# Performance work log

Hardware: AMD Instinct MI355X
Metric: run time of the kernel (lower is better)

The kernel has to match this reference:

```python
import jax, jax.numpy as jnp
import numpy as np


def setup_inputs() -> dict:
    key = jax.random.key(0)
    k1, k2 = jax.random.split(key)
    B, C, H, W = 32, 2, 512, 512
    inp = jax.random.normal(k1, (B, C, H, W), dtype=jnp.float32)
    tgt = jax.random.normal(k2, (B, C, H, W), dtype=jnp.float32)
    return {"input": inp, "target": tgt}


def reference(input, target):
    B, C, H, W = input.shape
    # normalized coordinate grids: (j+1)/W along x, (p+1)/H along y
    xg = jnp.arange(1, W + 1, dtype=input.dtype) / W  # (W,)
    yg = jnp.arange(1, H + 1, dtype=input.dtype) / H  # (H,)
    # softmax over flattened heatmap per (b, c)
    p = jax.nn.softmax(input.reshape(B, C, H * W), axis=-1).reshape(B, C, H, W)
    # soft-argmax coords in normalized units, then scaled to pixels (*W, *H)
    pred_x = jnp.einsum('bchw,w->bc', p, xg) * W
    pred_y = jnp.einsum('bchw,h->bc', p, yg) * H
    # ground truth: hard argmax of target heatmap -> pixel coords
    idx = jnp.argmax(target.reshape(B, C, H * W), axis=-1)
    true_x = (idx % W + 1).astype(input.dtype)   # ((idx%W+1)/W)*W
    true_y = (idx // W + 1).astype(input.dtype)  # ((idx//W+1)/H)*H
    ed = jnp.sqrt((true_x - pred_x) ** 2 + (true_y - pred_y) ** 2)  # (B, C)
    s_i = jnp.sum(ed[:, 0])   # channel 0 -> inferior
    s_s = jnp.sum(ed[:, 1:])  # remaining channels -> superior
    denom = jnp.asarray(B, input.dtype)
    return (s_i / denom, s_s / denom, (s_i + s_s) / denom)
```

## Files before the change

kernel.cpp:

```cpp
#include <hip/hip_runtime.h>
#include <math.h>

constexpr int Wd      = 512;
constexpr int Hd      = 512;
constexpr int HW      = Wd * Hd;
constexpr int NBC     = 64;
constexpr int SPLITS  = 32;
constexpr int CHUNK   = HW / SPLITS;
constexpr int NPART   = NBC * SPLITS;
constexpr int THREADS = 256;
constexpr int F4_PER_T = CHUNK / 4 / THREADS;


__global__ __launch_bounds__(THREADS) void dsnt_pass1(
    const float* __restrict__ inp, const float* __restrict__ tgt,
    float* __restrict__ ws) {
  const int bid   = blockIdx.x;
  const int role  = bid >> 11;
  const int sub   = bid & 2047;
  const int bc    = sub >> 5;
  const int split = sub & (SPLITS - 1);
  const int t     = threadIdx.x;
  const int rbase = split * CHUNK;

  __shared__ float sm0[4], sm1[4], sm2[4];
  __shared__ int   smi[4];
  const int wave = t >> 6;

  float* Pl = ws;
  float* Px = ws + NPART;
  float* Py = ws + 2 * NPART;
  float* Pv = ws + 3 * NPART;
  int*   Pi = (int*)(ws + 4 * NPART);

  if (role == 0) {
    const float4* ip4 = (const float4*)(inp + (size_t)bc * HW + (size_t)rbase);
    float4 a[F4_PER_T];
#pragma unroll
    for (int i = 0; i < F4_PER_T; ++i) a[i] = ip4[t + i * THREADS];

    float lA = 0.f, lB = 0.f, sxA = 0.f, sxB = 0.f, syA = 0.f, syB = 0.f;
#pragma unroll
    for (int i = 0; i < F4_PER_T; ++i) {
      const int r = rbase + (t + i * THREADS) * 4;
      const float yc = (float)((r >> 9) + 1);
      const float x0 = (float)((r & 511) + 1);
      const float e0 = __expf(a[i].x);
      const float e1 = __expf(a[i].y);
      const float e2 = __expf(a[i].z);
      const float e3 = __expf(a[i].w);
      lA += e0 + e2;
      lB += e1 + e3;
      sxA = fmaf(e0, x0,       sxA);  sxA = fmaf(e2, x0 + 2.f, sxA);
      sxB = fmaf(e1, x0 + 1.f, sxB);  sxB = fmaf(e3, x0 + 3.f, sxB);
      syA = fmaf(e0 + e2, yc, syA);
      syB = fmaf(e1 + e3, yc, syB);
    }
    float l = lA + lB, sx = sxA + sxB, sy = syA + syB;

#pragma unroll
    for (int off = 32; off; off >>= 1) {
      l  += __shfl_xor(l, off);
      sx += __shfl_xor(sx, off);
      sy += __shfl_xor(sy, off);
    }
    if ((t & 63) == 0) { sm0[wave] = l; sm1[wave] = sx; sm2[wave] = sy; }
    __syncthreads();
    if (t == 0) {
#pragma unroll
      for (int wv = 1; wv < 4; ++wv) { l += sm0[wv]; sx += sm1[wv]; sy += sm2[wv]; }
      Pl[sub] = l; Px[sub] = sx; Py[sub] = sy;
    }
  } else {
    const float4* tp4 = (const float4*)(tgt + (size_t)bc * HW + (size_t)rbase);
    float4 b[F4_PER_T];
#pragma unroll
    for (int i = 0; i < F4_PER_T; ++i) b[i] = tp4[t + i * THREADS];

    float tvA = -INFINITY, tvB = -INFINITY;
    int   tiA = 0, tiB = 0;
#pragma unroll
    for (int i = 0; i < F4_PER_T; ++i) {
      const int r = rbase + (t + i * THREADS) * 4;
      if (b[i].x > tvA) { tvA = b[i].x; tiA = r; }
      if (b[i].z > tvA) { tvA = b[i].z; tiA = r + 2; }
      if (b[i].y > tvB) { tvB = b[i].y; tiB = r + 1; }
      if (b[i].w > tvB) { tvB = b[i].w; tiB = r + 3; }
    }
    float tv = tvA; int ti = tiA;
    if (tvB > tv || (tvB == tv && tiB < ti)) { tv = tvB; ti = tiB; }

#pragma unroll
    for (int off = 32; off; off >>= 1) {
      const float tv2 = __shfl_xor(tv, off);
      const int   ti2 = __shfl_xor(ti, off);
      if (tv2 > tv || (tv2 == tv && ti2 < ti)) { tv = tv2; ti = ti2; }
    }
    if ((t & 63) == 0) { sm0[wave] = tv; smi[wave] = ti; }
    __syncthreads();
    if (t == 0) {
#pragma unroll
      for (int wv = 1; wv < 4; ++wv) {
        const float tv2 = sm0[wv];
        const int   ti2 = smi[wv];
        if (tv2 > tv || (tv2 == tv && ti2 < ti)) { tv = tv2; ti = ti2; }
      }
      Pv[sub] = tv; Pi[sub] = ti;
    }
  }
}

__global__ __launch_bounds__(256) void dsnt_pass2(const float* __restrict__ ws,
                                                  float* __restrict__ out) {
  const int t    = threadIdx.x;
  const int bc   = t >> 2;
  const int part = t & 3;
  const float* Pl = ws;
  const float* Px = ws + NPART;
  const float* Py = ws + 2 * NPART;
  const float* Pv = ws + 3 * NPART;
  const int*   Pi = (const int*)(ws + 4 * NPART);

  float l = 0.f, sx = 0.f, sy = 0.f;
  float tv = -INFINITY;
  int   ti = 0x7fffffff;
#pragma unroll
  for (int j = 0; j < 8; ++j) {
    const int p = bc * SPLITS + part * 8 + j;
    l  += Pl[p];
    sx += Px[p];
    sy += Py[p];
    const float v  = Pv[p];
    const int   ix = Pi[p];
    if (v > tv || (v == tv && ix < ti)) { tv = v; ti = ix; }
  }
#pragma unroll
  for (int off = 1; off <= 2; off <<= 1) {
    l  += __shfl_xor(l, off);
    sx += __shfl_xor(sx, off);
    sy += __shfl_xor(sy, off);
    const float tv2 = __shfl_xor(tv, off);
    const int   ti2 = __shfl_xor(ti, off);
    if (tv2 > tv || (tv2 == tv && ti2 < ti)) { tv = tv2; ti = ti2; }
  }

  __shared__ float edArr[NBC];
  if (part == 0) {
    const float predx = sx / l;
    const float predy = sy / l;
    const float truex = (float)((ti & 511) + 1);
    const float truey = (float)((ti >> 9) + 1);
    const float dx = truex - predx, dy = truey - predy;
    edArr[bc] = sqrtf(dx * dx + dy * dy);
  }
  __syncthreads();
  if (t < NBC) {
    const float ed = edArr[t];
    float ei = (t & 1) ? 0.f : ed;
    float es = (t & 1) ? ed : 0.f;
#pragma unroll
    for (int off = 32; off; off >>= 1) {
      ei += __shfl_xor(ei, off);
      es += __shfl_xor(es, off);
    }
    if (t == 0) {
      out[0] = ei * (1.f / 32.f);
      out[1] = es * (1.f / 32.f);
      out[2] = (ei + es) * (1.f / 32.f);
    }
  }
}

extern "C" void kernel_launch(void* const* d_in, const int* in_sizes, int n_in,
                              void* d_out, int out_size, void* d_ws, size_t ws_size,
                              hipStream_t stream) {
  const float* inp = (const float*)d_in[0];
  const float* tgt = (const float*)d_in[1];
  float* out = (float*)d_out;
  float* ws  = (float*)d_ws;

  dsnt_pass1<<<2 * NPART, THREADS, 0, stream>>>(inp, tgt, ws);
  dsnt_pass2<<<1, 256, 0, stream>>>(ws, out);
}
```

Baseline: 148.0 us.

## Stream pass1 through LDS with double-buffered direct global-to-LDS loads per wave

Each wave now owns an 8192-element segment and streams it through a per-wave double buffer in LDS using global_load_lds, with manual waitcnt to overlap the next chunk's load with compute on the current one. Each wave writes its own partial result, so the block-level shared reduction and barrier go away, and the grid shrinks to 1024 blocks. The aim is more bytes in flight per wave and fewer, larger work items, at the cost of hand-coded waitcnt encodings that depend on correct ordering.

```diff
diff --git a/kernel.cpp b/kernel.cpp
--- a/kernel.cpp
+++ b/kernel.cpp
@@ -5,27 +5,47 @@
 constexpr int Hd      = 512;
 constexpr int HW      = Wd * Hd;
 constexpr int NBC     = 64;
-constexpr int SPLITS  = 32;
-constexpr int CHUNK   = HW / SPLITS;
+constexpr int SEG     = 8192;
+constexpr int SPLITS  = HW / SEG;
 constexpr int NPART   = NBC * SPLITS;
 constexpr int THREADS = 256;
-constexpr int F4_PER_T = CHUNK / 4 / THREADS;
+constexpr int CHUNKF  = 1024;
+constexpr int NCHUNK  = SEG / CHUNKF;
 
+
+typedef __attribute__((address_space(1))) const void gvoid_t;
+typedef __attribute__((address_space(3))) void lvoid_t;
+
+#define WAIT_VM4()   __builtin_amdgcn_s_waitcnt(0x0F74)
+#define WAIT_VM0()   __builtin_amdgcn_s_waitcnt(0x0F70)
+#define WAIT_LGKM0() __builtin_amdgcn_s_waitcnt(0xC07F)
+
+__device__ __forceinline__ void stage_chunk(const float* __restrict__ g,
+                                            float* l, int lane) {
+#pragma unroll
+  for (int j = 0; j < 4; ++j) {
+    __builtin_amdgcn_global_load_lds((gvoid_t*)(g + j * 256 + lane * 4),
+                                     (lvoid_t*)(l + j * 256), 16, 0, 0);
+  }
+}
 
 __global__ __launch_bounds__(THREADS) void dsnt_pass1(
     const float* __restrict__ inp, const float* __restrict__ tgt,
     float* __restrict__ ws) {
-  const int bid   = blockIdx.x;
-  const int role  = bid >> 11;
-  const int sub   = bid & 2047;
-  const int bc    = sub >> 5;
-  const int split = sub & (SPLITS - 1);
-  const int t     = threadIdx.x;
-  const int rbase = split * CHUNK;
+  __shared__ __align__(16) float lds[2][4][CHUNKF];
+  const int t    = threadIdx.x;
+  const int lane = t & 63;
+  const int wv   = t >> 6;
+  const int bid  = blockIdx.x;
+  const int role = bid >> 9;
+  const int wid  = ((bid & 511) << 2) | wv;
+  const int bc    = wid >> 5;
+  const int split = wid & (SPLITS - 1);
+  const int hbase = split * SEG;
 
-  __shared__ float sm0[4], sm1[4], sm2[4];
-  __shared__ int   smi[4];
-  const int wave = t >> 6;
+  const float* src = (role == 0 ? inp : tgt) + (size_t)bc * HW + hbase;
+  float* lbuf0 = &lds[0][wv][0];
+  float* lbuf1 = &lds[1][wv][0];
 
   float* Pl = ws;
   float* Px = ws + NPART;
@@ -33,80 +53,75 @@
   float* Pv = ws + 3 * NPART;
   int*   Pi = (int*)(ws + 4 * NPART);
 
+  stage_chunk(src, lbuf0, lane);
+  stage_chunk(src + CHUNKF, lbuf1, lane);
+
   if (role == 0) {
-    const float4* ip4 = (const float4*)(inp + (size_t)bc * HW + (size_t)rbase);
-    float4 a[F4_PER_T];
-#pragma unroll
-    for (int i = 0; i < F4_PER_T; ++i) a[i] = ip4[t + i * THREADS];
-
     float lA = 0.f, lB = 0.f, sxA = 0.f, sxB = 0.f, syA = 0.f, syB = 0.f;
 #pragma unroll
-    for (int i = 0; i < F4_PER_T; ++i) {
-      const int r = rbase + (t + i * THREADS) * 4;
-      const float yc = (float)((r >> 9) + 1);
-      const float x0 = (float)((r & 511) + 1);
-      const float e0 = __expf(a[i].x);
-      const float e1 = __expf(a[i].y);
-      const float e2 = __expf(a[i].z);
-      const float e3 = __expf(a[i].w);
-      lA += e0 + e2;
-      lB += e1 + e3;
-      sxA = fmaf(e0, x0,       sxA);  sxA = fmaf(e2, x0 + 2.f, sxA);
-      sxB = fmaf(e1, x0 + 1.f, sxB);  sxB = fmaf(e3, x0 + 3.f, sxB);
-      syA = fmaf(e0 + e2, yc, syA);
-      syB = fmaf(e1 + e3, yc, syB);
+    for (int c = 0; c < NCHUNK; ++c) {
+      if (c < NCHUNK - 1) WAIT_VM4(); else WAIT_VM0();
+      const float4* lb4 = (const float4*)((c & 1) ? lbuf1 : lbuf0);
+#pragma unroll
+      for (int k = 0; k < 4; ++k) {
+        const float4 a = lb4[k * 64 + lane];
+        const int h = hbase + c * CHUNKF + k * 256 + lane * 4;
+        const float yc = (float)((h >> 9) + 1);
+        const float x0 = (float)((h & 511) + 1);
+        const float e0 = __expf(a.x);
+        const float e1 = __expf(a.y);
+        const float e2 = __expf(a.z);
+        const float e3 = __expf(a.w);
+        lA += e0 + e2;
+        lB += e1 + e3;
+        sxA = fmaf(e0, x0,       sxA);  sxA = fmaf(e2, x0 + 2.f, sxA);
+        sxB = fmaf(e1, x0 + 1.f, sxB);  sxB = fmaf(e3, x0 + 3.f, sxB);
+        syA = fmaf(e0 + e2, yc, syA);
+        syB = fmaf(e1 + e3, yc, syB);
+      }
+      if (c < NCHUNK - 2) {
+        WAIT_LGKM0();
+        stage_chunk(src + (c + 2) * CHUNKF, (c & 1) ? lbuf1 : lbuf0, lane);
+      }
     }
     float l = lA + lB, sx = sxA + sxB, sy = syA + syB;
-
 #pragma unroll
     for (int off = 32; off; off >>= 1) {
       l  += __shfl_xor(l, off);
       sx += __shfl_xor(sx, off);
       sy += __shfl_xor(sy, off);
     }
-    if ((t & 63) == 0) { sm0[wave] = l; sm1[wave] = sx; sm2[wave] = sy; }
-    __syncthreads();
-    if (t == 0) {
-#pragma unroll
-      for (int wv = 1; wv < 4; ++wv) { l += sm0[wv]; sx += sm1[wv]; sy += sm2[wv]; }
-      Pl[sub] = l; Px[sub] = sx; Py[sub] = sy;
-    }
+    if (lane == 0) { Pl[wid] = l; Px[wid] = sx; Py[wid] = sy; }
   } else {
-    const float4* tp4 = (const float4*)(tgt + (size_t)bc * HW + (size_t)rbase);
-    float4 b[F4_PER_T];
-#pragma unroll
-    for (int i = 0; i < F4_PER_T; ++i) b[i] = tp4[t + i * THREADS];
-
     float tvA = -INFINITY, tvB = -INFINITY;
     int   tiA = 0, tiB = 0;
 #pragma unroll
-    for (int i = 0; i < F4_PER_T; ++i) {
-      const int r = rbase + (t + i * THREADS) * 4;
-      if (b[i].x > tvA) { tvA = b[i].x; tiA = r; }
-      if (b[i].z > tvA) { tvA = b[i].z; tiA = r + 2; }
-      if (b[i].y > tvB) { tvB = b[i].y; tiB = r + 1; }
-      if (b[i].w > tvB) { tvB = b[i].w; tiB = r + 3; }
+    for (int c = 0; c < NCHUNK; ++c) {
+      if (c < NCHUNK - 1) WAIT_VM4(); else WAIT_VM0();
+      const float4* lb4 = (const float4*)((c & 1) ? lbuf1 : lbuf0);
+#pragma unroll
+      for (int k = 0; k < 4; ++k) {
+        const float4 b = lb4[k * 64 + lane];
+        const int h = hbase + c * CHUNKF + k * 256 + lane * 4;
+        if (b.x > tvA) { tvA = b.x; tiA = h; }
+        if (b.z > tvA) { tvA = b.z; tiA = h + 2; }
+        if (b.y > tvB) { tvB = b.y; tiB = h + 1; }
+        if (b.w > tvB) { tvB = b.w; tiB = h + 3; }
+      }
+      if (c < NCHUNK - 2) {
+        WAIT_LGKM0();
+        stage_chunk(src + (c + 2) * CHUNKF, (c & 1) ? lbuf1 : lbuf0, lane);
+      }
     }
     float tv = tvA; int ti = tiA;
     if (tvB > tv || (tvB == tv && tiB < ti)) { tv = tvB; ti = tiB; }
-
 #pragma unroll
     for (int off = 32; off; off >>= 1) {
       const float tv2 = __shfl_xor(tv, off);
       const int   ti2 = __shfl_xor(ti, off);
       if (tv2 > tv || (tv2 == tv && ti2 < ti)) { tv = tv2; ti = ti2; }
     }
-    if ((t & 63) == 0) { sm0[wave] = tv; smi[wave] = ti; }
-    __syncthreads();
-    if (t == 0) {
-#pragma unroll
-      for (int wv = 1; wv < 4; ++wv) {
-        const float tv2 = sm0[wv];
-        const int   ti2 = smi[wv];
-        if (tv2 > tv || (tv2 == tv && ti2 < ti)) { tv = tv2; ti = ti2; }
-      }
-      Pv[sub] = tv; Pi[sub] = ti;
-    }
+    if (lane == 0) { Pv[wid] = tv; Pi[wid] = ti; }
   }
 }
 
@@ -179,6 +194,6 @@
   float* out = (float*)d_out;
   float* ws  = (float*)d_ws;
 
-  dsnt_pass1<<<2 * NPART, THREADS, 0, stream>>>(inp, tgt, ws);
+  dsnt_pass1<<<1024, THREADS, 0, stream>>>(inp, tgt, ws);
   dsnt_pass2<<<1, 256, 0, stream>>>(ws, out);
 }
```

Measured after the change: 148.3 us. About the same (+0.2%).
